# Performance work log

Hardware: AMD Instinct MI355X
Metric: run time of the kernel (lower is better)

The kernel has to match this reference:

```python
import jax, jax.numpy as jnp
import numpy as np

MARGIN = 1.0


def setup_inputs() -> dict:
    key = jax.random.key(0)
    k1, k2 = jax.random.split(key)
    B, D = 8192, 128
    embedding = jax.random.normal(k1, (B, D), dtype=jnp.float32)
    target = jax.random.randint(k2, (B,), 0, 64, dtype=jnp.int64)
    return {"embedding": embedding, "target": target}


def reference(embedding, target):
    B = embedding.shape[0]
    # Pairwise Euclidean distances (cdist), used only for mining -> no grad.
    sq = jnp.sum(embedding * embedding, axis=1)                       # [B]
    d2 = sq[:, None] + sq[None, :] - 2.0 * (embedding @ embedding.T)  # [B, B]
    dist = jnp.sqrt(jnp.maximum(d2, 0.0))
    dist = jax.lax.stop_gradient(dist)

    same = target[:, None] == target[None, :]                         # [B, B]
    not_self = ~jnp.eye(B, dtype=bool)
    pos_mask = same & not_self
    neg_mask = ~same

    # Batch-hard mining: hardest (farthest) positive, hardest (closest) negative.
    pos_idx = jnp.argmax(jnp.where(pos_mask, dist, -jnp.inf), axis=1)  # [B]
    neg_idx = jnp.argmin(jnp.where(neg_mask, dist, jnp.inf), axis=1)   # [B]

    a = embedding
    p = embedding[pos_idx]
    n = embedding[neg_idx]

    dp = jnp.linalg.norm(a - p, axis=1)  # [B]
    dn = jnp.linalg.norm(a - n, axis=1)  # [B]
    loss = jax.nn.relu(dp - dn + MARGIN)
    return jnp.mean(loss)
```

## Files before the change

### kernel.cpp

```cpp
#include <hip/hip_runtime.h>
#include <hip/hip_bf16.h>
#include <math.h>

#define BN 8192
#define DK 128
#define NSPLIT 16
#define JR (BN / NSPLIT)
#define NG (JR / 128)
#define MARGIN_F 1.0f

#define OFF_EBS  524288
#define OFF_SQ   1048576
#define OFF_POSV (OFF_SQ + BN)
#define OFF_NEGV (OFF_POSV + NSPLIT * BN)
#define OFF_RED  (OFF_NEGV + NSPLIT * BN)

typedef __attribute__((ext_vector_type(8))) short bf16x8;
typedef __attribute__((ext_vector_type(4))) float f32x4;

__device__ __forceinline__ unsigned short f2bf(float f) {
    __hip_bfloat16 h = __float2bfloat16(f);
    return *reinterpret_cast<unsigned short*>(&h);
}

__device__ __forceinline__ void gload_lds16(const void* g, void* s) {
    __builtin_amdgcn_global_load_lds(
        (const __attribute__((address_space(1))) void*)g,
        (__attribute__((address_space(3))) void*)s, 16, 0, 0);
}

__global__ __launch_bounds__(256) void k_prep(const float* __restrict__ emb,
                                              unsigned short* __restrict__ Eb,
                                              unsigned short* __restrict__ EbS,
                                              float* __restrict__ sq64,
                                              unsigned long long* __restrict__ red) {
    if (blockIdx.x == 0 && threadIdx.x == 0) {
        red[0] = 0ULL;
        red[1] = 0ULL;
    }
    int row  = blockIdx.x * 4 + (threadIdx.x >> 6);
    int lane = threadIdx.x & 63;
    float2 v = ((const float2*)(emb + (size_t)row * DK))[lane];
    ushort2 o;  o.x  = f2bf(v.x);           o.y  = f2bf(v.y);
    ushort2 os; os.x = f2bf(v.x * -128.0f); os.y = f2bf(v.y * -128.0f);
    ((ushort2*)(Eb  + (size_t)row * DK))[lane] = o;
    ((ushort2*)(EbS + (size_t)row * DK))[lane] = os;
    float s = v.x * v.x + v.y * v.y;
    #pragma unroll
    for (int m = 32; m; m >>= 1) s += __shfl_xor(s, m);
    if (lane == 0) sq64[row] = 64.0f * s;
}

__global__ __launch_bounds__(256)
void k_mine8(const unsigned short* __restrict__ Eb,
             const unsigned short* __restrict__ EbS,
             const float* __restrict__ sq64,
             const int* __restrict__ tgt,
             float* __restrict__ posV, float* __restrict__ negV) {
    __shared__ __align__(16) char Blds[2][2][16384];

    const int tid = threadIdx.x;
    const int w   = tid >> 6;
    const int l   = tid & 63;
    const int lh  = l >> 4;
    const int tx  = l & 15;
    const int igroup = blockIdx.x >> 4;
    const int split  = blockIdx.x & 15;
    const int i0w = igroup * 256 + w * 64;
    const int jb  = split * JR;
    const char* EbB = (const char*)Eb;

    bf16x8 A[4][4];
    #pragma unroll
    for (int mi = 0; mi < 4; ++mi) {
        const char* rp = (const char*)EbS + (size_t)(i0w + mi * 16 + tx) * 256 + lh * 16;
        #pragma unroll
        for (int ks = 0; ks < 4; ++ks)
            A[mi][ks] = *(const bf16x8*)(rp + ks * 64);
    }

    int t8[16];
    #pragma unroll
    for (int mi = 0; mi < 4; ++mi) {
        int4 q = *(const int4*)(tgt + i0w + mi * 16 + lh * 4);
        t8[mi * 4 + 0] = q.x; t8[mi * 4 + 1] = q.y;
        t8[mi * 4 + 2] = q.z; t8[mi * 4 + 3] = q.w;
    }

    float pp[16], nn[16];
    #pragma unroll
    for (int r = 0; r < 16; ++r) { pp[r] = -INFINITY; nn[r] = INFINITY; }

    auto stage64 = [&](char* dst, int jcol0) {
        const char* S = EbB + (size_t)jcol0 * 256;
        #pragma unroll
        for (int q = 0; q < 4; ++q) {
            int f  = tid + 256 * q;
            int gr = f >> 4;
            int sc = (f & 15) ^ (gr & 7);
            gload_lds16(S + gr * 256 + sc * 16, dst + w * 1024 + q * 4096);
        }
    };

    stage64(Blds[0][0], jb);
    stage64(Blds[0][1], jb + 64);
    __syncthreads();

    for (int g = 0; g < NG; ++g) {
        const int buf = g & 1;
        if (g + 1 < NG) {
            stage64(Blds[buf ^ 1][0], jb + (g + 1) * 128);
            stage64(Blds[buf ^ 1][1], jb + (g + 1) * 128 + 64);
        }
        const int j0 = jb + g * 128;

        float sqv[4][2]; int tjv[4][2];
        #pragma unroll
        for (int s = 0; s < 4; ++s)
            #pragma unroll
            for (int u = 0; u < 2; ++u) {
                int j = j0 + s * 32 + u * 16 + tx;
                sqv[s][u] = sq64[j]; tjv[s][u] = tgt[j];
            }

        #pragma unroll
        for (int s = 0; s < 4; ++s) {
            f32x4 acc[4][2];
            #pragma unroll
            for (int mi = 0; mi < 4; ++mi)
                #pragma unroll
                for (int u = 0; u < 2; ++u) {
                    float sv = sqv[s][u];
                    f32x4 a0 = {sv, sv, sv, sv};
                    acc[mi][u] = a0;
                }

            const char* base = Blds[buf][s >> 1];
            #pragma unroll
            for (int ks = 0; ks < 4; ++ks) {
                bf16x8 Bf[2];
                #pragma unroll
                for (int u = 0; u < 2; ++u) {
                    int row = (s & 1) * 32 + u * 16 + tx;
                    int c   = (ks * 4 + lh) ^ (row & 7);
                    Bf[u] = *(const bf16x8*)(base + row * 256 + c * 16);
                }
                __builtin_amdgcn_s_setprio(1);
                #pragma unroll
                for (int mi = 0; mi < 4; ++mi)
                    #pragma unroll
                    for (int u = 0; u < 2; ++u)
                        acc[mi][u] = __builtin_amdgcn_mfma_f32_16x16x32_bf16(
                            A[mi][ks], Bf[u], acc[mi][u], 0, 0, 0);
                __builtin_amdgcn_s_setprio(0);
            }

            const int tj0 = tjv[s][0], tj1 = tjv[s][1];
            #pragma unroll
            for (int mi = 0; mi < 4; ++mi) {
                #pragma unroll
                for (int v = 0; v < 4; ++v) {
                    const int r = mi * 4 + v;
                    const int trg = t8[r];
                    float k0 = acc[mi][0][v];
                    float k1 = acc[mi][1][v];
                    bool s0 = (tj0 == trg);
                    bool s1 = (tj1 == trg);
                    float a0 = s0 ? k0 : -INFINITY;
                    float b0 = s0 ? INFINITY : k0;
                    float a1 = s1 ? k1 : -INFINITY;
                    float b1 = s1 ? INFINITY : k1;
                    pp[r] = fmaxf(fmaxf(pp[r], a0), a1);
                    nn[r] = fminf(fminf(nn[r], b0), b1);
                }
            }
        }

        __syncthreads();
    }

    #pragma unroll
    for (int r = 0; r < 16; ++r) {
        float p = pp[r], n = nn[r];
        #pragma unroll
        for (int m = 1; m < 16; m <<= 1) {
            p = fmaxf(p, __shfl_xor(p, m));
            n = fminf(n, __shfl_xor(n, m));
        }
        if (tx == 0) {
            int row = i0w + (r >> 2) * 16 + lh * 4 + (r & 3);
            posV[split * BN + row] = p;
            negV[split * BN + row] = n;
        }
    }
}

__global__ __launch_bounds__(256) void k_finm(const float* __restrict__ sq64,
                                              const float* __restrict__ posV,
                                              const float* __restrict__ negV,
                                              unsigned long long* __restrict__ red,
                                              float* __restrict__ out) {
    int row  = blockIdx.x * 256 + threadIdx.x;
    int lane = threadIdx.x & 63;

    float p = -INFINITY, n = INFINITY;
    #pragma unroll
    for (int s = 0; s < NSPLIT; ++s) {
        p = fmaxf(p, posV[s * BN + row]);
        n = fminf(n, negV[s * BN + row]);
    }
    float s64 = sq64[row];
    float d2p = fmaxf(p + s64, 0.f) * 0.015625f;
    float d2n = fmaxf(n + s64, 0.f) * 0.015625f;
    float lo  = sqrtf(d2p) - sqrtf(d2n) + MARGIN_F;
    lo = lo > 0.f ? lo : 0.f;

    #pragma unroll
    for (int m = 32; m; m >>= 1) lo += __shfl_xor(lo, m);
    __shared__ float part[4];
    if (lane == 0) part[threadIdx.x >> 6] = lo;
    __syncthreads();
    if (threadIdx.x == 0) {
        float bs = part[0] + part[1] + part[2] + part[3];
        atomicAdd(red, (unsigned long long)(bs * 16777216.0f));
        __threadfence();
        unsigned int t = atomicAdd((unsigned int*)(red + 1), 1u);
        if (t == gridDim.x - 1) {
            unsigned long long tot = atomicAdd(red, 0ULL);
            out[0] = (float)((double)tot / 16777216.0 / (double)BN);
        }
    }
}

extern "C" void kernel_launch(void* const* d_in, const int* in_sizes, int n_in,
                              void* d_out, int out_size, void* d_ws, size_t ws_size,
                              hipStream_t stream) {
    const float* emb = (const float*)d_in[0];
    const int*   tgt = (const int*)d_in[1];
    float* out = (float*)d_out;

    float* wsf = (float*)d_ws;
    unsigned short* Eb  = (unsigned short*)wsf;
    unsigned short* EbS = (unsigned short*)(wsf + OFF_EBS);
    float* sq64 = wsf + OFF_SQ;
    float* posV = wsf + OFF_POSV;
    float* negV = wsf + OFF_NEGV;
    unsigned long long* red = (unsigned long long*)(wsf + OFF_RED);

    k_prep<<<BN / 4, 256, 0, stream>>>(emb, Eb, EbS, sq64, red);
    k_mine8<<<(BN / 256) * NSPLIT, 256, 0, stream>>>(Eb, EbS, sq64, tgt, posV, negV);
    k_finm<<<BN / 256, 256, 0, stream>>>(sq64, posV, negV, red, out);
}
```

Baseline: 40.74 us.

## Load B fragments directly from global into registers with double buffering

The mining kernel stops staging column tiles through LDS with async global-to-LDS loads and block-wide barriers. Each wave now loads its B fragments, squared norms and targets straight from global memory into registers, double-buffered so the next 32-column slice is prefetched while the current one runs on MFMA. This removes LDS traffic and __syncthreads, but the four waves of a block now each fetch the same B data on their own, relying on cache, and register pressure goes up.

After: 57.99 us. +42.3%, slower.

```diff
diff --git a/kernel.cpp b/kernel.cpp
--- a/kernel.cpp
+++ b/kernel.cpp
@@ -6,7 +6,7 @@
 #define DK 128
 #define NSPLIT 16
 #define JR (BN / NSPLIT)
-#define NG (JR / 128)
+#define NSUB (JR / 32)
 #define MARGIN_F 1.0f
 
 #define OFF_EBS  524288
@@ -21,12 +21,6 @@
 __device__ __forceinline__ unsigned short f2bf(float f) {
     __hip_bfloat16 h = __float2bfloat16(f);
     return *reinterpret_cast<unsigned short*>(&h);
-}
-
-__device__ __forceinline__ void gload_lds16(const void* g, void* s) {
-    __builtin_amdgcn_global_load_lds(
-        (const __attribute__((address_space(1))) void*)g,
-        (__attribute__((address_space(3))) void*)s, 16, 0, 0);
 }
 
 __global__ __launch_bounds__(256) void k_prep(const float* __restrict__ emb,
@@ -52,13 +46,11 @@
 }
 
 __global__ __launch_bounds__(256)
-void k_mine8(const unsigned short* __restrict__ Eb,
-             const unsigned short* __restrict__ EbS,
-             const float* __restrict__ sq64,
-             const int* __restrict__ tgt,
-             float* __restrict__ posV, float* __restrict__ negV) {
-    __shared__ __align__(16) char Blds[2][2][16384];
-
+void k_mine10(const unsigned short* __restrict__ Eb,
+              const unsigned short* __restrict__ EbS,
+              const float* __restrict__ sq64,
+              const int* __restrict__ tgt,
+              float* __restrict__ posV, float* __restrict__ negV) {
     const int tid = threadIdx.x;
     const int w   = tid >> 6;
     const int l   = tid & 63;
@@ -91,92 +83,72 @@
     #pragma unroll
     for (int r = 0; r < 16; ++r) { pp[r] = -INFINITY; nn[r] = INFINITY; }
 
-    auto stage64 = [&](char* dst, int jcol0) {
-        const char* S = EbB + (size_t)jcol0 * 256;
-        #pragma unroll
-        for (int q = 0; q < 4; ++q) {
-            int f  = tid + 256 * q;
-            int gr = f >> 4;
-            int sc = (f & 15) ^ (gr & 7);
-            gload_lds16(S + gr * 256 + sc * 16, dst + w * 1024 + q * 4096);
+    bf16x8 BA[2][4], BB[2][4];
+    float sqA[2], sqB[2]; int tjA[2], tjB[2];
+
+    auto loadB = [&](bf16x8 (&Bn)[2][4], float (&sqn)[2], int (&tjn)[2], int s) {
+        #pragma unroll
+        for (int u = 0; u < 2; ++u) {
+            int j = jb + s * 32 + u * 16 + tx;
+            const char* bp = EbB + (size_t)j * 256 + lh * 16;
+            #pragma unroll
+            for (int ks = 0; ks < 4; ++ks)
+                Bn[u][ks] = *(const bf16x8*)(bp + ks * 64);
+            sqn[u] = sq64[j];
+            tjn[u] = tgt[j];
         }
     };
 
-    stage64(Blds[0][0], jb);
-    stage64(Blds[0][1], jb + 64);
-    __syncthreads();
-
-    for (int g = 0; g < NG; ++g) {
-        const int buf = g & 1;
-        if (g + 1 < NG) {
-            stage64(Blds[buf ^ 1][0], jb + (g + 1) * 128);
-            stage64(Blds[buf ^ 1][1], jb + (g + 1) * 128 + 64);
-        }
-        const int j0 = jb + g * 128;
-
-        float sqv[4][2]; int tjv[4][2];
-        #pragma unroll
-        for (int s = 0; s < 4; ++s)
+    auto body = [&](bf16x8 (&Bc)[2][4], float (&sqc)[2], int (&tjc)[2],
+                    bf16x8 (&Bn)[2][4], float (&sqn)[2], int (&tjn)[2], int s) {
+        if (s + 1 < NSUB) loadB(Bn, sqn, tjn, s + 1);
+
+        f32x4 acc[4][2];
+        #pragma unroll
+        for (int mi = 0; mi < 4; ++mi)
             #pragma unroll
             for (int u = 0; u < 2; ++u) {
-                int j = j0 + s * 32 + u * 16 + tx;
-                sqv[s][u] = sq64[j]; tjv[s][u] = tgt[j];
+                float sv = sqc[u];
+                f32x4 a0 = {sv, sv, sv, sv};
+                acc[mi][u] = a0;
             }
 
-        #pragma unroll
-        for (int s = 0; s < 4; ++s) {
-            f32x4 acc[4][2];
+        __builtin_amdgcn_s_setprio(1);
+        #pragma unroll
+        for (int ks = 0; ks < 4; ++ks)
             #pragma unroll
             for (int mi = 0; mi < 4; ++mi)
                 #pragma unroll
-                for (int u = 0; u < 2; ++u) {
-                    float sv = sqv[s][u];
-                    f32x4 a0 = {sv, sv, sv, sv};
-                    acc[mi][u] = a0;
-                }
-
-            const char* base = Blds[buf][s >> 1];
-            #pragma unroll
-            for (int ks = 0; ks < 4; ++ks) {
-                bf16x8 Bf[2];
-                #pragma unroll
-                for (int u = 0; u < 2; ++u) {
-                    int row = (s & 1) * 32 + u * 16 + tx;
-                    int c   = (ks * 4 + lh) ^ (row & 7);
-                    Bf[u] = *(const bf16x8*)(base + row * 256 + c * 16);
-                }
-                __builtin_amdgcn_s_setprio(1);
-                #pragma unroll
-                for (int mi = 0; mi < 4; ++mi)
-                    #pragma unroll
-                    for (int u = 0; u < 2; ++u)
-                        acc[mi][u] = __builtin_amdgcn_mfma_f32_16x16x32_bf16(
-                            A[mi][ks], Bf[u], acc[mi][u], 0, 0, 0);
-                __builtin_amdgcn_s_setprio(0);
+                for (int u = 0; u < 2; ++u)
+                    acc[mi][u] = __builtin_amdgcn_mfma_f32_16x16x32_bf16(
+                        A[mi][ks], Bc[u][ks], acc[mi][u], 0, 0, 0);
+        __builtin_amdgcn_s_setprio(0);
+
+        const int tj0 = tjc[0], tj1 = tjc[1];
+        #pragma unroll
+        for (int mi = 0; mi < 4; ++mi) {
+            #pragma unroll
+            for (int v = 0; v < 4; ++v) {
+                const int r = mi * 4 + v;
+                const int trg = t8[r];
+                float k0 = acc[mi][0][v];
+                float k1 = acc[mi][1][v];
+                bool s0 = (tj0 == trg);
+                bool s1 = (tj1 == trg);
+                float a0 = s0 ? k0 : -INFINITY;
+                float b0 = s0 ? INFINITY : k0;
+                float a1 = s1 ? k1 : -INFINITY;
+                float b1 = s1 ? INFINITY : k1;
+                pp[r] = fmaxf(fmaxf(pp[r], a0), a1);
+                nn[r] = fminf(fminf(nn[r], b0), b1);
             }
-
-            const int tj0 = tjv[s][0], tj1 = tjv[s][1];
-            #pragma unroll
-            for (int mi = 0; mi < 4; ++mi) {
-                #pragma unroll
-                for (int v = 0; v < 4; ++v) {
-                    const int r = mi * 4 + v;
-                    const int trg = t8[r];
-                    float k0 = acc[mi][0][v];
-                    float k1 = acc[mi][1][v];
-                    bool s0 = (tj0 == trg);
-                    bool s1 = (tj1 == trg);
-                    float a0 = s0 ? k0 : -INFINITY;
-                    float b0 = s0 ? INFINITY : k0;
-                    float a1 = s1 ? k1 : -INFINITY;
-                    float b1 = s1 ? INFINITY : k1;
-                    pp[r] = fmaxf(fmaxf(pp[r], a0), a1);
-                    nn[r] = fminf(fminf(nn[r], b0), b1);
-                }
-            }
-        }
-
-        __syncthreads();
+        }
+    };
+
+    loadB(BA, sqA, tjA, 0);
+    for (int s = 0; s < NSUB; s += 2) {
+        body(BA, sqA, tjA, BB, sqB, tjB, s);
+        body(BB, sqB, tjB, BA, sqA, tjA, s + 1);
     }
 
     #pragma unroll
@@ -248,6 +220,6 @@
     unsigned long long* red = (unsigned long long*)(wsf + OFF_RED);
 
     k_prep<<<BN / 4, 256, 0, stream>>>(emb, Eb, EbS, sq64, red);
-    k_mine8<<<(BN / 256) * NSPLIT, 256, 0, stream>>>(Eb, EbS, sq64, tgt, posV, negV);
+    k_mine10<<<(BN / 256) * NSPLIT, 256, 0, stream>>>(Eb, EbS, sq64, tgt, posV, negV);
     k_finm<<<BN / 256, 256, 0, stream>>>(sq64, posV, negV, red, out);
 }
```

## Shrink mining tile to 16 rows per wave for higher occupancy

Applied to the files above, without the earlier changes.

Reduces each wave's anchor tile from 64 to 16 rows and the per-iteration column tile from 128 to 64, quadrupling the grid and cutting register and LDS use so more blocks fit per CU. Target labels for a wave's rows are packed into one int as bytes. This aims to fix low occupancy from the small previous grid, at the cost of four times more B-tile loads per MFMA and less register reuse. Byte-packing assumes labels fit in 8 bits.

Result: slower. 44.42 us (+9.0%).

```diff
diff --git a/kernel.cpp b/kernel.cpp
--- a/kernel.cpp
+++ b/kernel.cpp
@@ -6,7 +6,7 @@
 #define DK 128
 #define NSPLIT 16
 #define JR (BN / NSPLIT)
-#define NG (JR / 128)
+#define NI (JR / 64)
 #define MARGIN_F 1.0f
 
 #define OFF_EBS  524288
@@ -51,45 +51,42 @@
     if (lane == 0) sq64[row] = 64.0f * s;
 }
 
-__global__ __launch_bounds__(256)
-void k_mine8(const unsigned short* __restrict__ Eb,
-             const unsigned short* __restrict__ EbS,
-             const float* __restrict__ sq64,
-             const int* __restrict__ tgt,
-             float* __restrict__ posV, float* __restrict__ negV) {
-    __shared__ __align__(16) char Blds[2][2][16384];
+__global__ __launch_bounds__(256, 4)
+void k_mine11(const unsigned short* __restrict__ Eb,
+              const unsigned short* __restrict__ EbS,
+              const float* __restrict__ sq64,
+              const int* __restrict__ tgt,
+              float* __restrict__ posV, float* __restrict__ negV) {
+    __shared__ __align__(16) char Blds[2][16384];
 
     const int tid = threadIdx.x;
     const int w   = tid >> 6;
     const int l   = tid & 63;
     const int lh  = l >> 4;
     const int tx  = l & 15;
-    const int igroup = blockIdx.x >> 4;
-    const int split  = blockIdx.x & 15;
-    const int i0w = igroup * 256 + w * 64;
+    const int rowgroup = blockIdx.x >> 4;
+    const int split    = blockIdx.x & 15;
+    const int i0w = rowgroup * 64 + w * 16;
     const int jb  = split * JR;
     const char* EbB = (const char*)Eb;
 
-    bf16x8 A[4][4];
-    #pragma unroll
-    for (int mi = 0; mi < 4; ++mi) {
-        const char* rp = (const char*)EbS + (size_t)(i0w + mi * 16 + tx) * 256 + lh * 16;
+    bf16x8 A[4];
+    {
+        const char* rp = (const char*)EbS + (size_t)(i0w + tx) * 256 + lh * 16;
         #pragma unroll
         for (int ks = 0; ks < 4; ++ks)
-            A[mi][ks] = *(const bf16x8*)(rp + ks * 64);
-    }
-
-    int t8[16];
-    #pragma unroll
-    for (int mi = 0; mi < 4; ++mi) {
-        int4 q = *(const int4*)(tgt + i0w + mi * 16 + lh * 4);
-        t8[mi * 4 + 0] = q.x; t8[mi * 4 + 1] = q.y;
-        t8[mi * 4 + 2] = q.z; t8[mi * 4 + 3] = q.w;
-    }
-
-    float pp[16], nn[16];
-    #pragma unroll
-    for (int r = 0; r < 16; ++r) { pp[r] = -INFINITY; nn[r] = INFINITY; }
+            A[ks] = *(const bf16x8*)(rp + ks * 64);
+    }
+
+    int tpk;
+    {
+        int4 q = *(const int4*)(tgt + i0w + lh * 4);
+        tpk = q.x | (q.y << 8) | (q.z << 16) | (q.w << 24);
+    }
+
+    float pp[4], nn[4];
+    #pragma unroll
+    for (int r = 0; r < 4; ++r) { pp[r] = -INFINITY; nn[r] = INFINITY; }
 
     auto stage64 = [&](char* dst, int jcol0) {
         const char* S = EbB + (size_t)jcol0 * 256;
@@ -102,77 +99,52 @@
         }
     };
 
-    stage64(Blds[0][0], jb);
-    stage64(Blds[0][1], jb + 64);
+    stage64(Blds[0], jb);
     __syncthreads();
 
-    for (int g = 0; g < NG; ++g) {
+    for (int g = 0; g < NI; ++g) {
         const int buf = g & 1;
-        if (g + 1 < NG) {
-            stage64(Blds[buf ^ 1][0], jb + (g + 1) * 128);
-            stage64(Blds[buf ^ 1][1], jb + (g + 1) * 128 + 64);
-        }
-        const int j0 = jb + g * 128;
-
-        float sqv[4][2]; int tjv[4][2];
-        #pragma unroll
-        for (int s = 0; s < 4; ++s)
-            #pragma unroll
-            for (int u = 0; u < 2; ++u) {
-                int j = j0 + s * 32 + u * 16 + tx;
-                sqv[s][u] = sq64[j]; tjv[s][u] = tgt[j];
-            }
-
-        #pragma unroll
-        for (int s = 0; s < 4; ++s) {
-            f32x4 acc[4][2];
-            #pragma unroll
-            for (int mi = 0; mi < 4; ++mi)
-                #pragma unroll
-                for (int u = 0; u < 2; ++u) {
-                    float sv = sqv[s][u];
-                    f32x4 a0 = {sv, sv, sv, sv};
-                    acc[mi][u] = a0;
-                }
-
-            const char* base = Blds[buf][s >> 1];
+        if (g + 1 < NI) stage64(Blds[buf ^ 1], jb + (g + 1) * 64);
+        const int j0 = jb + g * 64;
+        const char* base = Blds[buf];
+
+        #pragma unroll
+        for (int s = 0; s < 2; ++s) {
+            float sq0 = sq64[j0 + s * 32 + tx];
+            float sq1 = sq64[j0 + s * 32 + 16 + tx];
+            int   tj0 = tgt[j0 + s * 32 + tx];
+            int   tj1 = tgt[j0 + s * 32 + 16 + tx];
+
+            f32x4 acc0 = {sq0, sq0, sq0, sq0};
+            f32x4 acc1 = {sq1, sq1, sq1, sq1};
+
             #pragma unroll
             for (int ks = 0; ks < 4; ++ks) {
-                bf16x8 Bf[2];
-                #pragma unroll
-                for (int u = 0; u < 2; ++u) {
-                    int row = (s & 1) * 32 + u * 16 + tx;
-                    int c   = (ks * 4 + lh) ^ (row & 7);
-                    Bf[u] = *(const bf16x8*)(base + row * 256 + c * 16);
-                }
+                int row0 = s * 32 + tx;
+                int row1 = s * 32 + 16 + tx;
+                bf16x8 B0 = *(const bf16x8*)(base + row0 * 256 +
+                                             (((ks * 4 + lh) ^ (row0 & 7)) << 4));
+                bf16x8 B1 = *(const bf16x8*)(base + row1 * 256 +
+                                             (((ks * 4 + lh) ^ (row1 & 7)) << 4));
                 __builtin_amdgcn_s_setprio(1);
-                #pragma unroll
-                for (int mi = 0; mi < 4; ++mi)
-                    #pragma unroll
-                    for (int u = 0; u < 2; ++u)
-                        acc[mi][u] = __builtin_amdgcn_mfma_f32_16x16x32_bf16(
-                            A[mi][ks], Bf[u], acc[mi][u], 0, 0, 0);
+                acc0 = __builtin_amdgcn_mfma_f32_16x16x32_bf16(A[ks], B0, acc0, 0, 0, 0);
+                acc1 = __builtin_amdgcn_mfma_f32_16x16x32_bf16(A[ks], B1, acc1, 0, 0, 0);
                 __builtin_amdgcn_s_setprio(0);
             }
 
-            const int tj0 = tjv[s][0], tj1 = tjv[s][1];
             #pragma unroll
-            for (int mi = 0; mi < 4; ++mi) {
-                #pragma unroll
-                for (int v = 0; v < 4; ++v) {
-                    const int r = mi * 4 + v;
-                    const int trg = t8[r];
-                    float k0 = acc[mi][0][v];
-                    float k1 = acc[mi][1][v];
-                    bool s0 = (tj0 == trg);
-                    bool s1 = (tj1 == trg);
-                    float a0 = s0 ? k0 : -INFINITY;
-                    float b0 = s0 ? INFINITY : k0;
-                    float a1 = s1 ? k1 : -INFINITY;
-                    float b1 = s1 ? INFINITY : k1;
-                    pp[r] = fmaxf(fmaxf(pp[r], a0), a1);
-                    nn[r] = fminf(fminf(nn[r], b0), b1);
-                }
+            for (int r = 0; r < 4; ++r) {
+                const int trg = (tpk >> (8 * r)) & 0xFF;
+                float k0 = acc0[r];
+                float k1 = acc1[r];
+                bool s0 = (tj0 == trg);
+                bool s1 = (tj1 == trg);
+                float a0 = s0 ? k0 : -INFINITY;
+                float b0 = s0 ? INFINITY : k0;
+                float a1 = s1 ? k1 : -INFINITY;
+                float b1 = s1 ? INFINITY : k1;
+                pp[r] = fmaxf(fmaxf(pp[r], a0), a1);
+                nn[r] = fminf(fminf(nn[r], b0), b1);
             }
         }
 
@@ -180,7 +152,7 @@
     }
 
     #pragma unroll
-    for (int r = 0; r < 16; ++r) {
+    for (int r = 0; r < 4; ++r) {
         float p = pp[r], n = nn[r];
         #pragma unroll
         for (int m = 1; m < 16; m <<= 1) {
@@ -188,7 +160,7 @@
             n = fminf(n, __shfl_xor(n, m));
         }
         if (tx == 0) {
-            int row = i0w + (r >> 2) * 16 + lh * 4 + (r & 3);
+            int row = i0w + lh * 4 + r;
             posV[split * BN + row] = p;
             negV[split * BN + row] = n;
         }
@@ -248,6 +220,6 @@
     unsigned long long* red = (unsigned long long*)(wsf + OFF_RED);
 
     k_prep<<<BN / 4, 256, 0, stream>>>(emb, Eb, EbS, sq64, red);
-    k_mine8<<<(BN / 256) * NSPLIT, 256, 0, stream>>>(Eb, EbS, sq64, tgt, posV, negV);
+    k_mine11<<<(BN / 64) * NSPLIT, 256, 0, stream>>>(Eb, EbS, sq64, tgt, posV, negV);
     k_finm<<<BN / 256, 256, 0, stream>>>(sq64, posV, negV, red, out);
 }
```
